# Performance work log

Hardware: AMD Instinct MI355X
Metric: run time of the kernel (lower is better)

## Reference

```python
import jax, jax.numpy as jnp
import numpy as np

BETA = 0.25
NUM_BOOKS = 8
CODEBOOK_SIZE = 1024
CODEBOOK_DIM = 128
INPUT_DIM = 512


def setup_inputs() -> dict:
    key = jax.random.key(0)
    ks = jax.random.split(key, 6)
    B, T = 16, 4096
    z = jax.random.normal(ks[0], (B, INPUT_DIM, T), dtype=jnp.float32)
    W_in = jax.random.normal(ks[1], (CODEBOOK_DIM, INPUT_DIM), dtype=jnp.float32) * (1.0 / np.sqrt(INPUT_DIM))
    b_in = jax.random.normal(ks[2], (CODEBOOK_DIM,), dtype=jnp.float32) * 0.01
    W_out = jax.random.normal(ks[3], (INPUT_DIM, CODEBOOK_DIM), dtype=jnp.float32) * (1.0 / np.sqrt(CODEBOOK_DIM))
    b_out = jax.random.normal(ks[4], (INPUT_DIM,), dtype=jnp.float32) * 0.01
    # codebooks init: uniform(-1/size, 1/size) as in _make_codebook
    codebooks = jax.random.uniform(ks[5], (NUM_BOOKS, CODEBOOK_SIZE, CODEBOOK_DIM),
                                   dtype=jnp.float32,
                                   minval=-1.0 / CODEBOOK_SIZE, maxval=1.0 / CODEBOOK_SIZE)
    return {"z": z, "W_in": W_in, "b_in": b_in, "W_out": W_out, "b_out": b_out, "codebooks": codebooks}


def reference(z, W_in, b_in, W_out, b_out, codebooks):
    # z: [B, D_in, T]; codebooks: [K_books, S, d]
    residual = z
    total_loss = jnp.float32(0.0)
    codes_list = []
    for i in range(codebooks.shape[0]):
        r = residual.transpose(0, 2, 1)                       # [B, T, D_in]
        z_proj = jnp.einsum('btD,dD->btd', r, W_in) + b_in    # [B, T, d]
        cb = codebooks[i]                                      # [S, d]
        # squared euclidean distance; argmin matches torch.cdist argmin
        d2 = (jnp.sum(z_proj * z_proj, axis=-1, keepdims=True)
              - 2.0 * jnp.einsum('btd,sd->bts', z_proj, cb)
              + jnp.sum(cb * cb, axis=-1))                    # [B, T, S]
        idx = jnp.argmin(d2, axis=-1)                          # [B, T]
        z_q_proj = cb[idx]                                     # [B, T, d] gather
        z_q_st = z_proj + jax.lax.stop_gradient(z_q_proj - z_proj)
        commit = jnp.mean((jax.lax.stop_gradient(z_q_proj) - z_proj) ** 2)
        cb_loss = jnp.mean((z_q_proj - jax.lax.stop_gradient(z_proj)) ** 2)
        total_loss = total_loss + cb_loss + BETA * commit
        z_q = (jnp.einsum('btd,Dd->btD', z_q_st, W_out) + b_out).transpose(0, 2, 1)  # [B, D_in, T]
        residual = residual - z_q
        codes_list.append(idx)
    z_quantized = z - residual
    codes = jnp.stack(codes_list, axis=1)                      # [B, num_books, T]
    return z_quantized, codes, total_loss
```

## Files before the change

kernel.cpp:

```cpp
#include <hip/hip_runtime.h>
#include <cstdint>

constexpr int NB   = 8;
constexpr int S    = 1024;
constexpr int CD   = 128;
constexpr int DIN  = 512;
constexpr int BATCH= 16;
constexpr int T    = 4096;
constexpr int NTOK = BATCH * T;
constexpr int FCAP = 24;
constexpr float MARGIN = 4e-3f;

typedef __attribute__((ext_vector_type(8))) short bf16x8;
typedef __attribute__((ext_vector_type(4))) float f32x4;

__device__ __forceinline__ unsigned short f2bf(float f) {
  unsigned int u = __float_as_uint(f);
  return (unsigned short)((u + 0x7fffu + ((u >> 16) & 1u)) >> 16);
}

__global__ __launch_bounds__(256) void cbn32_kernel(const float* __restrict__ cbs,
                                                    float* __restrict__ cbn32) {
  int row = blockIdx.x * 256 + threadIdx.x;
  if (row >= NB * S) return;
  const float4* r4 = reinterpret_cast<const float4*>(cbs + (size_t)row * CD);
  double s = 0.0;
  for (int q = 0; q < 32; ++q) {
    float4 v = r4[q];
    s += (double)v.x * v.x + (double)v.y * v.y + (double)v.z * v.z + (double)v.w * v.w;
  }
  cbn32[row] = (float)s;
}

__global__ __launch_bounds__(256) void cb16_kernel(const float* __restrict__ cbs,
                                                   unsigned short* __restrict__ cb16) {
  int i = blockIdx.x * 256 + threadIdx.x;
  if (i < NB * S * CD) cb16[i] = f2bf(cbs[i]);
}

__global__ __launch_bounds__(256) void p64t_kernel(const float* __restrict__ Win,
                                                   const float* __restrict__ Wout,
                                                   double* __restrict__ P64t) {
  int n = blockIdx.x * 256 + threadIdx.x;
  int k = n >> 7, d = n & 127;
  double s = 0.0;
  for (int D = 0; D < DIN; ++D)
    s = fma((double)Win[(size_t)d * DIN + D], (double)Wout[(size_t)D * CD + k], s);
  P64t[(size_t)k * CD + d] = s;
}

__global__ void cvec64_kernel(const float* __restrict__ Win,
                              const float* __restrict__ bout,
                              double* __restrict__ cvec64) {
  int d = threadIdx.x;
  double s = 0.0;
  for (int D = 0; D < DIN; ++D)
    s = fma((double)Win[(size_t)d * DIN + D], (double)bout[D], s);
  cvec64[d] = s;
}

__global__ void pcf_kernel(const float* __restrict__ cbs,
                           const double* __restrict__ P64t,
                           const double* __restrict__ cvec64,
                           float* __restrict__ PCF32) {
  const int s = blockIdx.x, book = blockIdx.y;
  const int d = threadIdx.x;
  const float* cr = cbs + ((size_t)book * S + s) * CD;
  double acc = 0.0;
  for (int k = 0; k < CD; ++k)
    acc = fma((double)cr[k], P64t[(size_t)k * CD + d], acc);
  PCF32[((size_t)book * S + s) * CD + d] = (float)(acc + cvec64[d]);
}

__global__ __launch_bounds__(256) void a32_kernel(const float* __restrict__ z,
                                                  const float* __restrict__ Win,
                                                  const float* __restrict__ bin,
                                                  float* __restrict__ Acur,
                                                  unsigned short* __restrict__ z16) {
  __shared__ __align__(16) float Al[32][132];
  __shared__ __align__(16) float Bl[32][68];
  const int tid = threadIdx.x;
  const int t0 = blockIdx.x * 64;
  const int b  = blockIdx.y;
  const int mx = tid & 15, nx = tid >> 4;
  float acc[8][4] = {};
  for (int kc = 0; kc < 16; ++kc) {
    __syncthreads();
#pragma unroll
    for (int rep = 0; rep < 4; ++rep) {
      int idx = rep * 256 + tid;
      int r = idx >> 3, q = idx & 7;
      float4 v = reinterpret_cast<const float4*>(Win)[(size_t)r * 128 + kc * 8 + q];
      Al[q * 4 + 0][r] = v.x; Al[q * 4 + 1][r] = v.y;
      Al[q * 4 + 2][r] = v.z; Al[q * 4 + 3][r] = v.w;
    }
#pragma unroll
    for (int rep = 0; rep < 2; ++rep) {
      int idx = rep * 256 + tid;
      int kk = idx >> 4, q = idx & 15;
      float4 v = reinterpret_cast<const float4*>(z + ((size_t)(b * DIN + kc * 32 + kk)) * T + t0)[q];
      *reinterpret_cast<float4*>(&Bl[kk][q * 4]) = v;
    }
    __syncthreads();
#pragma unroll
    for (int kk = 0; kk < 32; ++kk) {
      float4 a0 = *reinterpret_cast<const float4*>(&Al[kk][mx * 8]);
      float4 a1 = *reinterpret_cast<const float4*>(&Al[kk][mx * 8 + 4]);
      float4 bv = *reinterpret_cast<const float4*>(&Bl[kk][nx * 4]);
      float a[8] = {a0.x, a0.y, a0.z, a0.w, a1.x, a1.y, a1.z, a1.w};
      float bb[4] = {bv.x, bv.y, bv.z, bv.w};
#pragma unroll
      for (int u = 0; u < 8; ++u)
#pragma unroll
        for (int j = 0; j < 4; ++j) acc[u][j] = fmaf(a[u], bb[j], acc[u][j]);
    }
  }
#pragma unroll
  for (int u = 0; u < 8; ++u) {
    int d = mx * 8 + u;
    float bi = bin[d];
    size_t base = (size_t)d * NTOK + (size_t)b * T + t0 + nx * 4;
    float4 o = make_float4(acc[u][0] + bi, acc[u][1] + bi, acc[u][2] + bi, acc[u][3] + bi);
    *reinterpret_cast<float4*>(Acur + base) = o;
    unsigned int b0 = f2bf(o.x), b1 = f2bf(o.y), b2 = f2bf(o.z), b3 = f2bf(o.w);
    uint2 h; h.x = b0 | (b1 << 16); h.y = b2 | (b3 << 16);
    *reinterpret_cast<uint2*>(z16 + base) = h;
  }
}

template <bool LAST>
__global__ __launch_bounds__(256) void fused_kernel(
    float* __restrict__ Acur,
    unsigned short* __restrict__ z16,
    const unsigned short* __restrict__ cb16b,
    const float* __restrict__ cbb,
    const float* __restrict__ cbn32b,
    const float* __restrict__ PCFb,
    int* __restrict__ codes,
    double* __restrict__ lpartF,
    int book) {
  __shared__ __align__(16) unsigned char smemA[34816];
  __shared__ __align__(16) unsigned char smemB[17408];
  __shared__ float Cna[1024];
  __shared__ float gmin[64];
  __shared__ float wmin[4][64];
  __shared__ int   fcnt[64];
  __shared__ unsigned short fls[64][FCAP];
  __shared__ double lred[64];
  __shared__ int   scode[64];
  __shared__ int   ovn;

  auto cbL = reinterpret_cast<unsigned short(*)[136]>(smemA);
  auto ZtT = reinterpret_cast<unsigned short(*)[136]>(smemB);

  const int tid = threadIdx.x;
  const int tok0 = blockIdx.x * 64;
  const int wv = tid >> 6, ln = tid & 63;
  const int lr = ln & 15, lg = ln >> 4;

  for (int rep = 0; rep < 4; ++rep) {
    int idx = rep * 256 + tid;
    int k = idx >> 3, tg = idx & 7;
    bf16x8 v = *reinterpret_cast<const bf16x8*>(z16 + (size_t)k * NTOK + tok0 + tg * 8);
#pragma unroll
    for (int e = 0; e < 8; ++e) ZtT[tg * 8 + e][k] = (unsigned short)v[e];
  }
#pragma unroll
  for (int rep = 0; rep < 4; ++rep) Cna[rep * 256 + tid] = cbn32b[rep * 256 + tid];
  if (tid < 64) { gmin[tid] = 3.4e38f; fcnt[tid] = 0; }

  for (int c = 0; c < 8; ++c) {
    __syncthreads();
    for (int rep = 0; rep < 8; ++rep) {
      int idx = rep * 256 + tid;
      int s = idx >> 4, q = idx & 15;
      *reinterpret_cast<bf16x8*>(&cbL[s][q * 8]) =
          *reinterpret_cast<const bf16x8*>(cb16b + (size_t)(c * 128 + s) * 128 + q * 8);
    }
    __syncthreads();

    f32x4 acc[2][4];
#pragma unroll
    for (int ss = 0; ss < 2; ++ss)
#pragma unroll
      for (int ts = 0; ts < 4; ++ts) acc[ss][ts] = (f32x4){0.f, 0.f, 0.f, 0.f};
#pragma unroll
    for (int ks = 0; ks < 4; ++ks) {
      bf16x8 a0 = *reinterpret_cast<const bf16x8*>(&cbL[wv * 32 + lr][ks * 32 + lg * 8]);
      bf16x8 a1 = *reinterpret_cast<const bf16x8*>(&cbL[wv * 32 + 16 + lr][ks * 32 + lg * 8]);
      bf16x8 b0 = *reinterpret_cast<const bf16x8*>(&ZtT[lr][ks * 32 + lg * 8]);
      bf16x8 b1 = *reinterpret_cast<const bf16x8*>(&ZtT[16 + lr][ks * 32 + lg * 8]);
      bf16x8 b2 = *reinterpret_cast<const bf16x8*>(&ZtT[32 + lr][ks * 32 + lg * 8]);
      bf16x8 b3 = *reinterpret_cast<const bf16x8*>(&ZtT[48 + lr][ks * 32 + lg * 8]);
      acc[0][0] = __builtin_amdgcn_mfma_f32_16x16x32_bf16(a0, b0, acc[0][0], 0, 0, 0);
      acc[0][1] = __builtin_amdgcn_mfma_f32_16x16x32_bf16(a0, b1, acc[0][1], 0, 0, 0);
      acc[0][2] = __builtin_amdgcn_mfma_f32_16x16x32_bf16(a0, b2, acc[0][2], 0, 0, 0);
      acc[0][3] = __builtin_amdgcn_mfma_f32_16x16x32_bf16(a0, b3, acc[0][3], 0, 0, 0);
      acc[1][0] = __builtin_amdgcn_mfma_f32_16x16x32_bf16(a1, b0, acc[1][0], 0, 0, 0);
      acc[1][1] = __builtin_amdgcn_mfma_f32_16x16x32_bf16(a1, b1, acc[1][1], 0, 0, 0);
      acc[1][2] = __builtin_amdgcn_mfma_f32_16x16x32_bf16(a1, b2, acc[1][2], 0, 0, 0);
      acc[1][3] = __builtin_amdgcn_mfma_f32_16x16x32_bf16(a1, b3, acc[1][3], 0, 0, 0);
    }
#pragma unroll
    for (int ss = 0; ss < 2; ++ss)
#pragma unroll
      for (int ts = 0; ts < 4; ++ts)
#pragma unroll
        for (int r = 0; r < 4; ++r)
          acc[ss][ts][r] = fmaf(-2.f, acc[ss][ts][r],
                                Cna[c * 128 + wv * 32 + ss * 16 + lg * 4 + r]);
    float mts[4];
#pragma unroll
    for (int ts = 0; ts < 4; ++ts) {
      float m = acc[0][ts][0];
#pragma unroll
      for (int r = 1; r < 4; ++r) m = fminf(m, acc[0][ts][r]);
#pragma unroll
      for (int r = 0; r < 4; ++r) m = fminf(m, acc[1][ts][r]);
      m = fminf(m, __shfl_xor(m, 16));
      m = fminf(m, __shfl_xor(m, 32));
      mts[ts] = m;
    }
    if (lg == 0) {
#pragma unroll
      for (int ts = 0; ts < 4; ++ts) wmin[wv][ts * 16 + lr] = mts[ts];
    }
    __syncthreads();
    if (tid < 64) {
      float g = fminf(fminf(wmin[0][tid], wmin[1][tid]), fminf(wmin[2][tid], wmin[3][tid]));
      gmin[tid] = fminf(gmin[tid], g);
    }
  }
  __syncthreads();

  for (int c = 0; c < 8; ++c) {
    __syncthreads();
    for (int rep = 0; rep < 8; ++rep) {
      int idx = rep * 256 + tid;
      int s = idx >> 4, q = idx & 15;
      *reinterpret_cast<bf16x8*>(&cbL[s][q * 8]) =
          *reinterpret_cast<const bf16x8*>(cb16b + (size_t)(c * 128 + s) * 128 + q * 8);
    }
    __syncthreads();

    f32x4 acc[2][4];
#pragma unroll
    for (int ss = 0; ss < 2; ++ss)
#pragma unroll
      for (int ts = 0; ts < 4; ++ts) acc[ss][ts] = (f32x4){0.f, 0.f, 0.f, 0.f};
#pragma unroll
    for (int ks = 0; ks < 4; ++ks) {
      bf16x8 a0 = *reinterpret_cast<const bf16x8*>(&cbL[wv * 32 + lr][ks * 32 + lg * 8]);
      bf16x8 a1 = *reinterpret_cast<const bf16x8*>(&cbL[wv * 32 + 16 + lr][ks * 32 + lg * 8]);
      bf16x8 b0 = *reinterpret_cast<const bf16x8*>(&ZtT[lr][ks * 32 + lg * 8]);
      bf16x8 b1 = *reinterpret_cast<const bf16x8*>(&ZtT[16 + lr][ks * 32 + lg * 8]);
      bf16x8 b2 = *reinterpret_cast<const bf16x8*>(&ZtT[32 + lr][ks * 32 + lg * 8]);
      bf16x8 b3 = *reinterpret_cast<const bf16x8*>(&ZtT[48 + lr][ks * 32 + lg * 8]);
      acc[0][0] = __builtin_amdgcn_mfma_f32_16x16x32_bf16(a0, b0, acc[0][0], 0, 0, 0);
      acc[0][1] = __builtin_amdgcn_mfma_f32_16x16x32_bf16(a0, b1, acc[0][1], 0, 0, 0);
      acc[0][2] = __builtin_amdgcn_mfma_f32_16x16x32_bf16(a0, b2, acc[0][2], 0, 0, 0);
      acc[0][3] = __builtin_amdgcn_mfma_f32_16x16x32_bf16(a0, b3, acc[0][3], 0, 0, 0);
      acc[1][0] = __builtin_amdgcn_mfma_f32_16x16x32_bf16(a1, b0, acc[1][0], 0, 0, 0);
      acc[1][1] = __builtin_amdgcn_mfma_f32_16x16x32_bf16(a1, b1, acc[1][1], 0, 0, 0);
      acc[1][2] = __builtin_amdgcn_mfma_f32_16x16x32_bf16(a1, b2, acc[1][2], 0, 0, 0);
      acc[1][3] = __builtin_amdgcn_mfma_f32_16x16x32_bf16(a1, b3, acc[1][3], 0, 0, 0);
    }
#pragma unroll
    for (int ss = 0; ss < 2; ++ss)
#pragma unroll
      for (int ts = 0; ts < 4; ++ts)
#pragma unroll
        for (int r = 0; r < 4; ++r)
          acc[ss][ts][r] = fmaf(-2.f, acc[ss][ts][r],
                                Cna[c * 128 + wv * 32 + ss * 16 + lg * 4 + r]);
#pragma unroll
    for (int ts = 0; ts < 4; ++ts) {
      int t = ts * 16 + lr;
      float thr = gmin[t] + MARGIN;
#pragma unroll
      for (int ss = 0; ss < 2; ++ss)
#pragma unroll
        for (int r = 0; r < 4; ++r) {
          float v = acc[ss][ts][r];
          int s = c * 128 + wv * 32 + ss * 16 + lg * 4 + r;
          if (v <= thr) {
            int pos = atomicAdd(&fcnt[t], 1);
            if (pos < FCAP) fls[t][pos] = (unsigned short)s;
          }
        }
    }
  }
  __syncthreads();

  auto Zl   = reinterpret_cast<float(*)[64]>(smemA);
  auto znp  = reinterpret_cast<double(*)[64]>(smemB);
  float*  znl   = reinterpret_cast<float*>(smemB + 2048);
  auto bestv    = reinterpret_cast<float(*)[64]>(smemB + 2304);
  auto bests    = reinterpret_cast<int(*)[64]>(smemB + 3328);
  float*  rm    = reinterpret_cast<float*>(smemB + 4352);
  int*    ri    = reinterpret_cast<int*>(smemB + 5376);
  int*    ovl   = reinterpret_cast<int*>(smemB + 6400);
  unsigned char* ovf = smemB + 6656;

  const int b = tok0 >> 12;
  const int tl = tid & 63, h = tid >> 6;
  if (tid == 0) ovn = 0;
  for (int rep = 0; rep < 8; ++rep) {
    int idx = rep * 256 + tid;
    int d = idx >> 4, q = idx & 15;
    float4 v = *reinterpret_cast<const float4*>(Acur + (size_t)d * NTOK + tok0 + q * 4);
    Zl[d][q * 4 + 0] = v.x; Zl[d][q * 4 + 1] = v.y;
    Zl[d][q * 4 + 2] = v.z; Zl[d][q * 4 + 3] = v.w;
  }
  __syncthreads();
  {
    double s = 0.0;
#pragma unroll
    for (int dd = 0; dd < 32; ++dd) { double v = (double)Zl[h * 32 + dd][tl]; s += v * v; }
    znp[h][tl] = s;
  }
  __syncthreads();
  if (tid < 64) znl[tid] = (float)(((znp[0][tid] + znp[1][tid]) + znp[2][tid]) + znp[3][tid]);
  __syncthreads();
  const float zn = znl[tl];
  const int cnt = fcnt[tl];
  float bm = 3.4e38f; int bi = 0x7fffffff;
  if (cnt <= FCAP) {
    if (h == 0) ovf[tl] = 0;
    for (int i = h; i < cnt; i += 4) {
      int s = fls[tl][i];
      const float* cr = cbb + (size_t)s * CD;
      double e = 0.0;
      for (int d = 0; d < CD; ++d) e = fma((double)cr[d], (double)Zl[d][tl], e);
      float M = (float)e;
      float d2 = __fadd_rn(__fsub_rn(zn, __fmul_rn(2.f, M)), cbn32b[s]);
      if (d2 < bm || (d2 == bm && s < bi)) { bm = d2; bi = s; }
    }
  } else {
    if (h == 0) { int p = atomicAdd(&ovn, 1); ovl[p] = tl; ovf[tl] = 1; }
  }
  bestv[h][tl] = bm; bests[h][tl] = bi;
  __syncthreads();
  if (tid < 64 && !ovf[tid]) {
    float fv = bestv[0][tid]; int fs = bests[0][tid];
#pragma unroll
    for (int x = 1; x < 4; ++x) {
      float v = bestv[x][tid]; int s = bests[x][tid];
      if (v < fv || (v == fv && s < fs)) { fv = v; fs = s; }
    }
    codes[((size_t)b * NB + book) * T + ((tok0 + tid) & (T - 1))] = fs;
    scode[tid] = fs;
    lred[tid] = (double)fv;
  }
  __syncthreads();
  const int no = ovn;
  for (int e = 0; e < no; ++e) {
    const int tt = ovl[e];
    const float zn2 = znl[tt];
    double e0 = 0.0, e1 = 0.0, e2 = 0.0, e3 = 0.0;
    const float* c0 = cbb + (size_t)(tid      ) * CD;
    const float* c1 = cbb + (size_t)(tid + 256) * CD;
    const float* c2 = cbb + (size_t)(tid + 512) * CD;
    const float* c3 = cbb + (size_t)(tid + 768) * CD;
    for (int d = 0; d < CD; ++d) {
      double zv = (double)Zl[d][tt];
      e0 = fma((double)c0[d], zv, e0);
      e1 = fma((double)c1[d], zv, e1);
      e2 = fma((double)c2[d], zv, e2);
      e3 = fma((double)c3[d], zv, e3);
    }
    float bm2 = 3.4e38f; int bi2 = 0x7fffffff;
    {
      float d2;
      d2 = __fadd_rn(__fsub_rn(zn2, __fmul_rn(2.f, (float)e0)), cbn32b[tid]);
      if (d2 < bm2) { bm2 = d2; bi2 = tid; }
      d2 = __fadd_rn(__fsub_rn(zn2, __fmul_rn(2.f, (float)e1)), cbn32b[tid + 256]);
      if (d2 < bm2) { bm2 = d2; bi2 = tid + 256; }
      d2 = __fadd_rn(__fsub_rn(zn2, __fmul_rn(2.f, (float)e2)), cbn32b[tid + 512]);
      if (d2 < bm2) { bm2 = d2; bi2 = tid + 512; }
      d2 = __fadd_rn(__fsub_rn(zn2, __fmul_rn(2.f, (float)e3)), cbn32b[tid + 768]);
      if (d2 < bm2) { bm2 = d2; bi2 = tid + 768; }
    }
    rm[tid] = bm2; ri[tid] = bi2;
    __syncthreads();
    for (int off = 128; off; off >>= 1) {
      if (tid < off) {
        float om = rm[tid + off]; int oi = ri[tid + off];
        if (om < rm[tid] || (om == rm[tid] && oi < ri[tid])) { rm[tid] = om; ri[tid] = oi; }
      }
      __syncthreads();
    }
    if (tid == 0) {
      codes[((size_t)b * NB + book) * T + ((tok0 + tt) & (T - 1))] = ri[0];
      scode[tt] = ri[0];
      lred[tt] = (double)rm[0];
    }
    __syncthreads();
  }
  if (tid == 0) {
    double sum = 0.0;
    for (int i = 0; i < 64; ++i) sum += lred[i];
    lpartF[(size_t)book * 1024 + blockIdx.x] = sum;
  }

  if constexpr (!LAST) {
    __syncthreads();
    const int code = scode[tl];
    const float* pr = PCFb + (size_t)code * CD + h * 32;
#pragma unroll
    for (int d = 0; d < 32; ++d) {
      int dd = h * 32 + d;
      size_t idx = (size_t)dd * NTOK + tok0 + tl;
      float v = Zl[dd][tl] - pr[d];
      Acur[idx] = v;
      z16[idx] = f2bf(v);
    }
  }
}

__global__ __launch_bounds__(256) void qsgather_kernel(const float* __restrict__ cbs,
                                                       const int* __restrict__ codes,
                                                       float* __restrict__ qs32) {
  __shared__ int cds[64][8];
  const int tid = threadIdx.x;
  const int tok0 = blockIdx.x * 64;
  const int tl = tid & 63, h = tid >> 6;
  if (tid < 64) {
    int tok = tok0 + tid, b = tok >> 12, t = tok & (T - 1);
#pragma unroll
    for (int book = 0; book < NB; ++book)
      cds[tid][book] = codes[((size_t)b * NB + book) * T + t];
  }
  __syncthreads();
  const int tok = tok0 + tl;
  float acc[32] = {};
#pragma unroll
  for (int book = 0; book < NB; ++book) {
    const float* cr = cbs + ((size_t)book * S + cds[tl][book]) * CD + h * 32;
#pragma unroll
    for (int k = 0; k < 32; ++k) acc[k] += cr[k];
  }
#pragma unroll
  for (int k = 0; k < 32; ++k)
    qs32[(size_t)(h * 32 + k) * NTOK + tok] = acc[k];
}

__global__ __launch_bounds__(256) void final32_kernel(const float* __restrict__ qs32,
                                                      const float* __restrict__ Wout,
                                                      const float* __restrict__ bout,
                                                      float* __restrict__ out) {
  __shared__ __align__(16) float Al[32][132];
  __shared__ __align__(16) float Bl[32][68];
  const int tid = threadIdx.x;
  const int t0 = blockIdx.x * 64;
  const int Dg = blockIdx.y;
  const int b  = blockIdx.z;
  const int mx = tid & 15, nx = tid >> 4;
  const size_t tokbase = (size_t)b * T + t0;
  float acc[8][4] = {};
  for (int kc = 0; kc < 4; ++kc) {
    __syncthreads();
#pragma unroll
    for (int rep = 0; rep < 4; ++rep) {
      int idx = rep * 256 + tid;
      int r = idx >> 3, q = idx & 7;
      float4 v = reinterpret_cast<const float4*>(Wout)[(size_t)(Dg * 128 + r) * 32 + kc * 8 + q];
      Al[q * 4 + 0][r] = v.x; Al[q * 4 + 1][r] = v.y;
      Al[q * 4 + 2][r] = v.z; Al[q * 4 + 3][r] = v.w;
    }
#pragma unroll
    for (int rep = 0; rep < 2; ++rep) {
      int idx = rep * 256 + tid;
      int kk = idx >> 4, q = idx & 15;
      *reinterpret_cast<float4*>(&Bl[kk][q * 4]) =
          *reinterpret_cast<const float4*>(qs32 + (size_t)(kc * 32 + kk) * NTOK + tokbase + q * 4);
    }
    __syncthreads();
#pragma unroll
    for (int kk = 0; kk < 32; ++kk) {
      float4 a0 = *reinterpret_cast<const float4*>(&Al[kk][mx * 8]);
      float4 a1 = *reinterpret_cast<const float4*>(&Al[kk][mx * 8 + 4]);
      float4 bv = *reinterpret_cast<const float4*>(&Bl[kk][nx * 4]);
      float a[8] = {a0.x, a0.y, a0.z, a0.w, a1.x, a1.y, a1.z, a1.w};
      float bb[4] = {bv.x, bv.y, bv.z, bv.w};
#pragma unroll
      for (int u = 0; u < 8; ++u)
#pragma unroll
        for (int j = 0; j < 4; ++j) acc[u][j] = fmaf(a[u], bb[j], acc[u][j]);
    }
  }
#pragma unroll
  for (int u = 0; u < 8; ++u) {
    int D = Dg * 128 + mx * 8 + u;
    float bo = 8.0f * bout[D];
    float4 o = make_float4(acc[u][0] + bo, acc[u][1] + bo, acc[u][2] + bo, acc[u][3] + bo);
    reinterpret_cast<float4*>(out + ((size_t)b * DIN + D) * T + t0)[nx] = o;
  }
}

__global__ __launch_bounds__(256) void codes_out_kernel(const int* __restrict__ codes,
                                                        float* __restrict__ out) {
  int k = blockIdx.x * 256 + threadIdx.x;
  if (k < BATCH * NB * T)
    out[(size_t)BATCH * DIN * T + k] = (float)codes[k];
}

__global__ __launch_bounds__(256) void loss_out_kernel(const double* __restrict__ lpF,
                                                       float* __restrict__ out) {
  __shared__ double red[256];
  double s = 0.0;
  for (int i = threadIdx.x; i < NB * 1024; i += 256) s += lpF[i];
  red[threadIdx.x] = s;
  __syncthreads();
  for (int off = 128; off; off >>= 1) {
    if (threadIdx.x < off) red[threadIdx.x] += red[threadIdx.x + off];
    __syncthreads();
  }
  if (threadIdx.x == 0)
    out[(size_t)BATCH * DIN * T + (size_t)BATCH * NB * T] =
        (float)(red[0] * 1.25 / 8388608.0);
}

extern "C" void kernel_launch(void* const* d_in, const int* in_sizes, int n_in,
                              void* d_out, int out_size, void* d_ws, size_t ws_size,
                              hipStream_t stream) {
  (void)in_sizes; (void)n_in; (void)out_size; (void)ws_size;
  const float* z    = (const float*)d_in[0];
  const float* Win  = (const float*)d_in[1];
  const float* bin  = (const float*)d_in[2];
  const float* Wout = (const float*)d_in[3];
  const float* bout = (const float*)d_in[4];
  const float* cbs  = (const float*)d_in[5];
  float* out = (float*)d_out;
  float* Acur = out;

  char* w = (char*)d_ws;
  double* P64t  = (double*)w;  w += (size_t)CD * CD * 8;
  double* cvec64= (double*)w;  w += CD * 8;
  double* lpartF= (double*)w;  w += (size_t)NB * 1024 * 8;
  float*  PCF32 = (float*)w;   w += (size_t)NB * S * CD * 4;
  float*  qs32  = (float*)w;   w += (size_t)CD * NTOK * 4;
  float*  cbn32 = (float*)w;   w += (size_t)NB * S * 4;
  unsigned short* z16  = (unsigned short*)w; w += (size_t)CD * NTOK * 2;
  unsigned short* cb16 = (unsigned short*)w; w += (size_t)NB * S * CD * 2;
  int*    codes = (int*)w;     w += (size_t)BATCH * NB * T * 4;

  cbn32_kernel<<<(NB * S + 255) / 256, 256, 0, stream>>>(cbs, cbn32);
  cb16_kernel<<<(NB * S * CD + 255) / 256, 256, 0, stream>>>(cbs, cb16);
  p64t_kernel<<<64, 256, 0, stream>>>(Win, Wout, P64t);
  cvec64_kernel<<<1, 128, 0, stream>>>(Win, bout, cvec64);
  pcf_kernel<<<dim3(S, NB), 128, 0, stream>>>(cbs, P64t, cvec64, PCF32);
  a32_kernel<<<dim3(T / 64, BATCH), 256, 0, stream>>>(z, Win, bin, Acur, z16);

  for (int book = 0; book < NB; ++book) {
    const float* cb = cbs + (size_t)book * S * CD;
    const unsigned short* cbh = cb16 + (size_t)book * S * CD;
    if (book < NB - 1)
      fused_kernel<false><<<NTOK / 64, 256, 0, stream>>>(
          Acur, z16, cbh, cb, cbn32 + book * S,
          PCF32 + (size_t)book * S * CD, codes, lpartF, book);
    else
      fused_kernel<true><<<NTOK / 64, 256, 0, stream>>>(
          Acur, z16, cbh, cb, cbn32 + book * S,
          PCF32 + (size_t)book * S * CD, codes, lpartF, book);
  }
  qsgather_kernel<<<NTOK / 64, 256, 0, stream>>>(cbs, codes, qs32);
  final32_kernel<<<dim3(T / 64, DIN / 128, BATCH), 256, 0, stream>>>(qs32, Wout, bout, out);
  codes_out_kernel<<<(BATCH * NB * T + 255) / 256, 256, 0, stream>>>(codes, out);
  loss_out_kernel<<<1, 256, 0, stream>>>(lpartF, out);
}
```

Before: 1.218 ms.

## Collect argmin candidates in a single pass and pre-transpose projection weights

The fused kernel no longer recomputes codebook distances with a second bf16 MFMA sweep. Candidate codes are now filtered in the same chunk loop that updates the running per-token minimum, using the current running minimum plus a margin as the threshold. Because an early, looser threshold can admit more candidates, the candidate cap is raised from 24 to 32, with overflow handled by the existing fallback path. Separately, W_in and W_out are transposed once by small kernels, so the a32 and final GEMMs load weight tiles into shared memory with vector stores instead of scattered scalar transposing writes.

```diff
diff --git a/kernel.cpp b/kernel.cpp
--- a/kernel.cpp
+++ b/kernel.cpp
@@ -8,7 +8,7 @@
 constexpr int BATCH= 16;
 constexpr int T    = 4096;
 constexpr int NTOK = BATCH * T;
-constexpr int FCAP = 24;
+constexpr int FCAP = 32;
 constexpr float MARGIN = 4e-3f;
 
 typedef __attribute__((ext_vector_type(8))) short bf16x8;
@@ -72,8 +72,22 @@
   PCF32[((size_t)book * S + s) * CD + d] = (float)(acc + cvec64[d]);
 }
 
+__global__ __launch_bounds__(256) void winT_kernel(const float* __restrict__ Win,
+                                                   float* __restrict__ WinT) {
+  int i = blockIdx.x * 256 + threadIdx.x;
+  int D = i >> 7, d = i & 127;
+  WinT[(size_t)D * 128 + d] = Win[(size_t)d * 512 + D];
+}
+
+__global__ __launch_bounds__(256) void woutT_kernel(const float* __restrict__ Wout,
+                                                    float* __restrict__ WoutT) {
+  int i = blockIdx.x * 256 + threadIdx.x;
+  int k = i >> 9, D = i & 511;
+  WoutT[(size_t)k * 512 + D] = Wout[(size_t)D * 128 + k];
+}
+
 __global__ __launch_bounds__(256) void a32_kernel(const float* __restrict__ z,
-                                                  const float* __restrict__ Win,
+                                                  const float* __restrict__ WinT,
                                                   const float* __restrict__ bin,
                                                   float* __restrict__ Acur,
                                                   unsigned short* __restrict__ z16) {
@@ -89,10 +103,9 @@
 #pragma unroll
     for (int rep = 0; rep < 4; ++rep) {
       int idx = rep * 256 + tid;
-      int r = idx >> 3, q = idx & 7;
-      float4 v = reinterpret_cast<const float4*>(Win)[(size_t)r * 128 + kc * 8 + q];
-      Al[q * 4 + 0][r] = v.x; Al[q * 4 + 1][r] = v.y;
-      Al[q * 4 + 2][r] = v.z; Al[q * 4 + 3][r] = v.w;
+      int kk = idx >> 5, q = idx & 31;
+      float4 v = *reinterpret_cast<const float4*>(WinT + (size_t)(kc * 32 + kk) * 128 + q * 4);
+      *reinterpret_cast<float4*>(&Al[kk][q * 4]) = v;
     }
 #pragma unroll
     for (int rep = 0; rep < 2; ++rep) {
@@ -230,49 +243,7 @@
       float g = fminf(fminf(wmin[0][tid], wmin[1][tid]), fminf(wmin[2][tid], wmin[3][tid]));
       gmin[tid] = fminf(gmin[tid], g);
     }
-  }
-  __syncthreads();
-
-  for (int c = 0; c < 8; ++c) {
-    __syncthreads();
-    for (int rep = 0; rep < 8; ++rep) {
-      int idx = rep * 256 + tid;
-      int s = idx >> 4, q = idx & 15;
-      *reinterpret_cast<bf16x8*>(&cbL[s][q * 8]) =
-          *reinterpret_cast<const bf16x8*>(cb16b + (size_t)(c * 128 + s) * 128 + q * 8);
-    }
-    __syncthreads();
-
-    f32x4 acc[2][4];
-#pragma unroll
-    for (int ss = 0; ss < 2; ++ss)
-#pragma unroll
-      for (int ts = 0; ts < 4; ++ts) acc[ss][ts] = (f32x4){0.f, 0.f, 0.f, 0.f};
-#pragma unroll
-    for (int ks = 0; ks < 4; ++ks) {
-      bf16x8 a0 = *reinterpret_cast<const bf16x8*>(&cbL[wv * 32 + lr][ks * 32 + lg * 8]);
-      bf16x8 a1 = *reinterpret_cast<const bf16x8*>(&cbL[wv * 32 + 16 + lr][ks * 32 + lg * 8]);
-      bf16x8 b0 = *reinterpret_cast<const bf16x8*>(&ZtT[lr][ks * 32 + lg * 8]);
-      bf16x8 b1 = *reinterpret_cast<const bf16x8*>(&ZtT[16 + lr][ks * 32 + lg * 8]);
-      bf16x8 b2 = *reinterpret_cast<const bf16x8*>(&ZtT[32 + lr][ks * 32 + lg * 8]);
-      bf16x8 b3 = *reinterpret_cast<const bf16x8*>(&ZtT[48 + lr][ks * 32 + lg * 8]);
-      acc[0][0] = __builtin_amdgcn_mfma_f32_16x16x32_bf16(a0, b0, acc[0][0], 0, 0, 0);
-      acc[0][1] = __builtin_amdgcn_mfma_f32_16x16x32_bf16(a0, b1, acc[0][1], 0, 0, 0);
-      acc[0][2] = __builtin_amdgcn_mfma_f32_16x16x32_bf16(a0, b2, acc[0][2], 0, 0, 0);
-      acc[0][3] = __builtin_amdgcn_mfma_f32_16x16x32_bf16(a0, b3, acc[0][3], 0, 0, 0);
-      acc[1][0] = __builtin_amdgcn_mfma_f32_16x16x32_bf16(a1, b0, acc[1][0], 0, 0, 0);
-      acc[1][1] = __builtin_amdgcn_mfma_f32_16x16x32_bf16(a1, b1, acc[1][1], 0, 0, 0);
-      acc[1][2] = __builtin_amdgcn_mfma_f32_16x16x32_bf16(a1, b2, acc[1][2], 0, 0, 0);
-      acc[1][3] = __builtin_amdgcn_mfma_f32_16x16x32_bf16(a1, b3, acc[1][3], 0, 0, 0);
-    }
-#pragma unroll
-    for (int ss = 0; ss < 2; ++ss)
-#pragma unroll
-      for (int ts = 0; ts < 4; ++ts)
-#pragma unroll
-        for (int r = 0; r < 4; ++r)
-          acc[ss][ts][r] = fmaf(-2.f, acc[ss][ts][r],
-                                Cna[c * 128 + wv * 32 + ss * 16 + lg * 4 + r]);
+    __syncthreads();
 #pragma unroll
     for (int ts = 0; ts < 4; ++ts) {
       int t = ts * 16 + lr;
@@ -282,8 +253,8 @@
 #pragma unroll
         for (int r = 0; r < 4; ++r) {
           float v = acc[ss][ts][r];
-          int s = c * 128 + wv * 32 + ss * 16 + lg * 4 + r;
           if (v <= thr) {
+            int s = c * 128 + wv * 32 + ss * 16 + lg * 4 + r;
             int pos = atomicAdd(&fcnt[t], 1);
             if (pos < FCAP) fls[t][pos] = (unsigned short)s;
           }
@@ -446,7 +417,7 @@
 }
 
 __global__ __launch_bounds__(256) void final32_kernel(const float* __restrict__ qs32,
-                                                      const float* __restrict__ Wout,
+                                                      const float* __restrict__ WoutT,
                                                       const float* __restrict__ bout,
                                                       float* __restrict__ out) {
   __shared__ __align__(16) float Al[32][132];
@@ -463,10 +434,10 @@
 #pragma unroll
     for (int rep = 0; rep < 4; ++rep) {
       int idx = rep * 256 + tid;
-      int r = idx >> 3, q = idx & 7;
-      float4 v = reinterpret_cast<const float4*>(Wout)[(size_t)(Dg * 128 + r) * 32 + kc * 8 + q];
-      Al[q * 4 + 0][r] = v.x; Al[q * 4 + 1][r] = v.y;
-      Al[q * 4 + 2][r] = v.z; Al[q * 4 + 3][r] = v.w;
+      int kk = idx >> 5, q = idx & 31;
+      float4 v = *reinterpret_cast<const float4*>(
+          WoutT + (size_t)(kc * 32 + kk) * 512 + Dg * 128 + q * 4);
+      *reinterpret_cast<float4*>(&Al[kk][q * 4]) = v;
     }
 #pragma unroll
     for (int rep = 0; rep < 2; ++rep) {
@@ -541,6 +512,8 @@
   float*  PCF32 = (float*)w;   w += (size_t)NB * S * CD * 4;
   float*  qs32  = (float*)w;   w += (size_t)CD * NTOK * 4;
   float*  cbn32 = (float*)w;   w += (size_t)NB * S * 4;
+  float*  WinT  = (float*)w;   w += (size_t)DIN * CD * 4;
+  float*  WoutT = (float*)w;   w += (size_t)CD * DIN * 4;
   unsigned short* z16  = (unsigned short*)w; w += (size_t)CD * NTOK * 2;
   unsigned short* cb16 = (unsigned short*)w; w += (size_t)NB * S * CD * 2;
   int*    codes = (int*)w;     w += (size_t)BATCH * NB * T * 4;
@@ -550,7 +523,9 @@
   p64t_kernel<<<64, 256, 0, stream>>>(Win, Wout, P64t);
   cvec64_kernel<<<1, 128, 0, stream>>>(Win, bout, cvec64);
   pcf_kernel<<<dim3(S, NB), 128, 0, stream>>>(cbs, P64t, cvec64, PCF32);
-  a32_kernel<<<dim3(T / 64, BATCH), 256, 0, stream>>>(z, Win, bin, Acur, z16);
+  winT_kernel<<<256, 256, 0, stream>>>(Win, WinT);
+  woutT_kernel<<<256, 256, 0, stream>>>(Wout, WoutT);
+  a32_kernel<<<dim3(T / 64, BATCH), 256, 0, stream>>>(z, WinT, bin, Acur, z16);
 
   for (int book = 0; book < NB; ++book) {
     const float* cb = cbs + (size_t)book * S * CD;
@@ -565,7 +540,7 @@
           PCF32 + (size_t)book * S * CD, codes, lpartF, book);
   }
   qsgather_kernel<<<NTOK / 64, 256, 0, stream>>>(cbs, codes, qs32);
-  final32_kernel<<<dim3(T / 64, DIN / 128, BATCH), 256, 0, stream>>>(qs32, Wout, bout, out);
+  final32_kernel<<<dim3(T / 64, DIN / 128, BATCH), 256, 0, stream>>>(qs32, WoutT, bout, out);
   codes_out_kernel<<<(BATCH * NB * T + 255) / 256, 256, 0, stream>>>(codes, out);
   loss_out_kernel<<<1, 256, 0, stream>>>(lpartF, out);
 }
```

Measured after the change: 1.229 ms. No clear change (+0.9%).
